# Kernel tuning notes

Hardware: AMD Instinct MI355X
Metric: run time of the kernel (lower is better)

Reference implementation:

```python
import jax, jax.numpy as jnp
import numpy as np

DIM = 2048
N_HEADS = 16
N_KV = 4
HEAD_DIM = DIM // N_HEADS  # 128
G = N_HEADS // N_KV        # queries per kv head
EPS = 1e-6
ROPE_BASE = 10000.0


def _rms_norm(x, w):
    # x: [..., head_dim]
    norm = jax.lax.rsqrt(jnp.mean(x * x, axis=-1, keepdims=True) + EPS)
    return x * norm * w


def _rope_tables(seq_len, dtype):
    inv_freq = 1.0 / (ROPE_BASE ** (jnp.arange(0, HEAD_DIM, 2, dtype=jnp.float32) / HEAD_DIM))
    t = jnp.arange(seq_len, dtype=jnp.float32)
    freqs = jnp.einsum('i,j->ij', t, inv_freq)          # [S, hd/2]
    emb = jnp.concatenate([freqs, freqs], axis=-1)       # [S, hd]
    return jnp.cos(emb).astype(dtype), jnp.sin(emb).astype(dtype)


def _rotate_half(x):
    x1, x2 = x[..., : HEAD_DIM // 2], x[..., HEAD_DIM // 2:]
    return jnp.concatenate([-x2, x1], axis=-1)


def setup_inputs() -> dict:
    key = jax.random.key(0)
    ks = jax.random.split(key, 7)
    x = jax.random.normal(ks[0], (2, 2048, DIM), dtype=jnp.float32)
    s = 0.02
    Wq = jax.random.normal(ks[1], (DIM, DIM), dtype=jnp.float32) * s
    Wk = jax.random.normal(ks[2], (DIM, N_KV * HEAD_DIM), dtype=jnp.float32) * s
    Wv = jax.random.normal(ks[3], (DIM, N_KV * HEAD_DIM), dtype=jnp.float32) * s
    Wo = jax.random.normal(ks[4], (DIM, DIM), dtype=jnp.float32) * s
    q_norm_w = jnp.ones((HEAD_DIM,), dtype=jnp.float32)
    k_norm_w = jnp.ones((HEAD_DIM,), dtype=jnp.float32)
    return {"x": x, "Wq": Wq, "Wk": Wk, "Wv": Wv, "Wo": Wo,
            "q_norm_w": q_norm_w, "k_norm_w": k_norm_w}


def reference(x, Wq, Wk, Wv, Wo, q_norm_w, k_norm_w):
    B, S, _ = x.shape
    q = (x @ Wq).reshape(B, S, N_HEADS, HEAD_DIM)
    k = (x @ Wk).reshape(B, S, N_KV, HEAD_DIM)
    v = (x @ Wv).reshape(B, S, N_KV, HEAD_DIM)

    q = _rms_norm(q, q_norm_w)
    k = _rms_norm(k, k_norm_w)

    q = q.transpose(0, 2, 1, 3)  # [B, H, S, hd]
    k = k.transpose(0, 2, 1, 3)  # [B, KV, S, hd]
    v = v.transpose(0, 2, 1, 3)

    cos, sin = _rope_tables(S, x.dtype)  # [S, hd], broadcasts over B,H
    q = q * cos + _rotate_half(q) * sin
    k = k * cos + _rotate_half(k) * sin

    # GQA: group queries by kv head instead of repeating K/V (same math as repeat_interleave)
    qg = q.reshape(B, N_KV, G, S, HEAD_DIM)
    scale = HEAD_DIM ** -0.5
    scores = jnp.einsum('bkgqd,bkkd2->bkgqk2'.replace('k2', 'K').replace('d2', 'd'),
                        qg, k) if False else jnp.einsum('bkgqd,bkKd->bkgqK', qg, k) * scale
    attn = jax.nn.softmax(scores, axis=-1)               # [B, KV, G, S, S]
    out = jnp.einsum('bkgqK,bkKd->bkgqd', attn, v)       # [B, KV, G, S, hd]
    out = out.reshape(B, N_HEADS, S, HEAD_DIM).transpose(0, 2, 1, 3).reshape(B, S, DIM)
    return out @ Wo
```

## Files before the change

kernel.cpp:

```cpp
#include <hip/hip_runtime.h>
#include <stdint.h>

#define LOG2E 1.4426950408889634f

typedef __attribute__((ext_vector_type(8))) short short8;
typedef __attribute__((ext_vector_type(4))) float floatx4;
typedef unsigned int u32;

__device__ __forceinline__ float bf2f(unsigned short h) {
  union { unsigned int u; float f; } v; v.u = ((unsigned int)h) << 16; return v.f;
}
__device__ __forceinline__ unsigned short f2bf(float f) {
  union { float f; unsigned int u; } v; v.f = f;
  unsigned int r = v.u + 0x7FFFu + ((v.u >> 16) & 1u);
  return (unsigned short)(r >> 16);
}
__device__ __forceinline__ u32 fbits(float f) {
  union { float f; u32 u; } v; v.f = f; return v.u;
}
__device__ __forceinline__ void async16(void* lds, const void* g) {
  __builtin_amdgcn_global_load_lds((const __attribute__((address_space(1))) u32*)g,
                                   (__attribute__((address_space(3))) u32*)lds, 16, 0, 0);
}

__global__ __launch_bounds__(256) void prep1(const float* __restrict__ x,
                                             const float* __restrict__ Wq,
                                             const float* __restrict__ Wk,
                                             const float* __restrict__ Wv,
                                             const float* __restrict__ Wo,
                                             unsigned short* __restrict__ xbf,
                                             unsigned short* __restrict__ WTqkv,
                                             unsigned short* __restrict__ WoT) {
  __shared__ unsigned short tile[64][65];
  int bid = blockIdx.x;
  if (bid < 4096) {
    int i = (bid * 256 + threadIdx.x) * 8;
    float4 a = ((const float4*)(x + i))[0];
    float4 b = ((const float4*)(x + i))[1];
    union { uint4 v; unsigned short u[8]; } o;
    o.u[0] = f2bf(a.x); o.u[1] = f2bf(a.y); o.u[2] = f2bf(a.z); o.u[3] = f2bf(a.w);
    o.u[4] = f2bf(b.x); o.u[5] = f2bf(b.y); o.u[6] = f2bf(b.z); o.u[7] = f2bf(b.w);
    *(uint4*)(xbf + i) = o.v;
    return;
  }
  bid -= 4096;
  const int R = 2048;
  const float* src; unsigned short* dst; int C;
  if (bid < 1024) { src = Wq; dst = WTqkv; C = 2048; }
  else if (bid < 1280) { src = Wk; dst = WTqkv + (size_t)2048 * 2048; C = 512; bid -= 1024; }
  else if (bid < 1536) { src = Wv; dst = WTqkv + (size_t)2048 * 2048 + (size_t)512 * 2048; C = 512; bid -= 1280; }
  else { src = Wo; dst = WoT; C = 2048; bid -= 1536; }

  int tc = C >> 6;
  int br = bid / tc, bc = bid % tc;
  int r0 = br << 6, c0 = bc << 6;
  int i = threadIdx.x >> 2, cc = (threadIdx.x & 3) << 4;
  const float4* g = (const float4*)(src + (size_t)(r0 + i) * C + c0 + cc);
  float4 f0 = g[0], f1 = g[1], f2 = g[2], f3 = g[3];
  unsigned short u[16];
  u[0]=f2bf(f0.x); u[1]=f2bf(f0.y); u[2]=f2bf(f0.z); u[3]=f2bf(f0.w);
  u[4]=f2bf(f1.x); u[5]=f2bf(f1.y); u[6]=f2bf(f1.z); u[7]=f2bf(f1.w);
  u[8]=f2bf(f2.x); u[9]=f2bf(f2.y); u[10]=f2bf(f2.z); u[11]=f2bf(f2.w);
  u[12]=f2bf(f3.x); u[13]=f2bf(f3.y); u[14]=f2bf(f3.z); u[15]=f2bf(f3.w);
#pragma unroll
  for (int j = 0; j < 16; ++j) tile[i][cc + j] = u[j];
  __syncthreads();
  union { uint4 v[2]; unsigned short u[16]; } buf;
#pragma unroll
  for (int j = 0; j < 16; ++j) buf.u[j] = tile[cc + j][i];
  uint4* o = (uint4*)(dst + (size_t)(c0 + i) * R + r0 + cc);
  o[0] = buf.v[0]; o[1] = buf.v[1];
}

template <typename OutT>
__global__ __launch_bounds__(512, 2) void gemm_nt_256(const unsigned short* __restrict__ A,
                                                      const unsigned short* __restrict__ BT,
                                                      OutT* __restrict__ C,
                                                      int M, int N, int K) {
  (void)M;
  __shared__ unsigned short As[2][256 * 64];
  __shared__ unsigned short Bs[2][256 * 64];
  const int nbn = N >> 8;
  const int nwg = gridDim.x;
  int wg = blockIdx.x;
  {
    int cpx = nwg >> 3;
    wg = (wg & 7) * cpx + (wg >> 3);
  }
  const int m0 = (wg / nbn) << 8;
  const int n0 = (wg % nbn) << 8;
  const int tid = threadIdx.x;
  const int lane = tid & 63, wave = tid >> 6;
  const int l15 = lane & 15, quad = lane >> 4;
  const int wr = wave >> 2, wc = wave & 3;
  const int rA = wr * 128 + l15;
  const int rB = wc * 64 + l15;

  floatx4 acc[8][4];
#pragma unroll
  for (int i = 0; i < 8; ++i)
#pragma unroll
    for (int j = 0; j < 4; ++j) acc[i][j] = (floatx4){0.f, 0.f, 0.f, 0.f};

  const unsigned short* Ag = A + (size_t)m0 * K;
  const unsigned short* Bg = BT + (size_t)n0 * K;

  auto STAGE = [&](unsigned short* dst, const unsigned short* g, int h) {
#pragma unroll
    for (int j = 0; j < 2; ++j) {
      int idx = j * 512 + tid;
      int row = h * 128 + (idx >> 3);
      int cl = (idx & 7) ^ (row & 7);
      async16(dst + (size_t)h * 8192 + (size_t)idx * 8, g + (size_t)row * K + cl * 8);
    }
  };
  auto RD = [&](const unsigned short* buf, int row, int ks) -> short8 {
    int sc = ((ks << 2) + quad) ^ (row & 7);
    return *(const short8*)(buf + row * 64 + sc * 8);
  };

#define BAR() __builtin_amdgcn_s_barrier()
#define WAITL0() asm volatile("s_waitcnt lgkmcnt(0)" ::: "memory")

  STAGE(As[0], Ag, 0); STAGE(As[0], Ag, 1);
  STAGE(Bs[0], Bg, 0); STAGE(Bs[0], Bg, 1);
  STAGE(As[1], Ag + 64, 0); STAGE(As[1], Ag + 64, 1);
  asm volatile("s_waitcnt vmcnt(4)" ::: "memory");
  BAR();

  const int NT = K >> 6;
  short8 a0[4][2], a1[4][2], b0[2][2], b1[2][2];
  for (int t = 0; t < NT; ++t) {
    const unsigned short* Ac = As[t & 1];
    const unsigned short* Bc = Bs[t & 1];
    unsigned short* Ast = As[t & 1];
    unsigned short* Bst = Bs[(t + 1) & 1];

#pragma unroll
    for (int mf = 0; mf < 4; ++mf)
#pragma unroll
      for (int ks = 0; ks < 2; ++ks) a0[mf][ks] = RD(Ac, rA + mf * 16, ks);
#pragma unroll
    for (int nf = 0; nf < 2; ++nf)
#pragma unroll
      for (int ks = 0; ks < 2; ++ks) b0[nf][ks] = RD(Bc, rB + nf * 16, ks);
    if (t + 1 < NT) STAGE(Bst, Bg + (size_t)(t + 1) * 64, 0);
    asm volatile("s_waitcnt lgkmcnt(8)" ::: "memory");
    BAR(); WAITL0();
    __builtin_amdgcn_s_setprio(1);
#pragma unroll
    for (int mf = 0; mf < 4; ++mf)
#pragma unroll
      for (int nf = 0; nf < 2; ++nf)
#pragma unroll
        for (int ks = 0; ks < 2; ++ks)
          acc[mf][nf] = __builtin_amdgcn_mfma_f32_16x16x32_bf16(a0[mf][ks], b0[nf][ks], acc[mf][nf], 0, 0, 0);
    __builtin_amdgcn_s_setprio(0);
    BAR();

#pragma unroll
    for (int mf = 0; mf < 4; ++mf)
#pragma unroll
      for (int ks = 0; ks < 2; ++ks) a1[mf][ks] = RD(Ac, rA + 64 + mf * 16, ks);
    if (t + 1 < NT) STAGE(Bst, Bg + (size_t)(t + 1) * 64, 1);
    BAR(); WAITL0();
    __builtin_amdgcn_s_setprio(1);
#pragma unroll
    for (int mf = 0; mf < 4; ++mf)
#pragma unroll
      for (int nf = 0; nf < 2; ++nf)
#pragma unroll
        for (int ks = 0; ks < 2; ++ks)
          acc[4 + mf][nf] = __builtin_amdgcn_mfma_f32_16x16x32_bf16(a1[mf][ks], b0[nf][ks], acc[4 + mf][nf], 0, 0, 0);
    __builtin_amdgcn_s_setprio(0);
    BAR();

#pragma unroll
    for (int nf = 0; nf < 2; ++nf)
#pragma unroll
      for (int ks = 0; ks < 2; ++ks) b1[nf][ks] = RD(Bc, rB + 32 + nf * 16, ks);
    if (t + 2 < NT) STAGE(Ast, Ag + (size_t)(t + 2) * 64, 0);
    BAR(); WAITL0();
    __builtin_amdgcn_s_setprio(1);
#pragma unroll
    for (int mf = 0; mf < 4; ++mf)
#pragma unroll
      for (int nf = 0; nf < 2; ++nf)
#pragma unroll
        for (int ks = 0; ks < 2; ++ks)
          acc[4 + mf][2 + nf] = __builtin_amdgcn_mfma_f32_16x16x32_bf16(a1[mf][ks], b1[nf][ks], acc[4 + mf][2 + nf], 0, 0, 0);
    __builtin_amdgcn_s_setprio(0);
    BAR();

    if (t + 2 < NT) {
      STAGE(Ast, Ag + (size_t)(t + 2) * 64, 1);
      asm volatile("s_waitcnt vmcnt(4)" ::: "memory");
    } else {
      asm volatile("s_waitcnt vmcnt(0)" ::: "memory");
    }
    BAR();
    __builtin_amdgcn_s_setprio(1);
#pragma unroll
    for (int mf = 0; mf < 4; ++mf)
#pragma unroll
      for (int nf = 0; nf < 2; ++nf)
#pragma unroll
        for (int ks = 0; ks < 2; ++ks)
          acc[mf][2 + nf] = __builtin_amdgcn_mfma_f32_16x16x32_bf16(a0[mf][ks], b1[nf][ks], acc[mf][2 + nf], 0, 0, 0);
    __builtin_amdgcn_s_setprio(0);
    BAR();
  }
#undef BAR
#undef WAITL0

#pragma unroll
  for (int mf = 0; mf < 8; ++mf)
#pragma unroll
    for (int nf = 0; nf < 4; ++nf)
#pragma unroll
      for (int r = 0; r < 4; ++r) {
        int m = m0 + wr * 128 + mf * 16 + quad * 4 + r;
        int n = n0 + wc * 64 + nf * 16 + l15;
        float v = acc[mf][nf][r];
        if constexpr (sizeof(OutT) == 2)
          C[(size_t)m * N + n] = (OutT)f2bf(v);
        else
          C[(size_t)m * N + n] = (OutT)v;
      }
}

__global__ __launch_bounds__(512, 2) void gemm_nt_128x256(const unsigned short* __restrict__ A,
                                                          const unsigned short* __restrict__ BT,
                                                          float* __restrict__ C,
                                                          int M, int N, int K) {
  (void)M;
  __shared__ unsigned short As[2][128 * 64];
  __shared__ unsigned short Bs[2][256 * 64];
  const int nbn = N >> 8;
  const int nwg = gridDim.x;
  int wg = blockIdx.x;
  {
    int cpx = nwg >> 3;
    wg = (wg & 7) * cpx + (wg >> 3);
  }
  const int m0 = (wg / nbn) << 7;
  const int n0 = (wg % nbn) << 8;
  const int tid = threadIdx.x;
  const int lane = tid & 63, wave = tid >> 6;
  const int l15 = lane & 15, quad = lane >> 4;
  const int wr = wave >> 2, wc = wave & 3;
  const int rA = wr * 64 + l15;
  const int rB = wc * 64 + l15;

  floatx4 acc[4][4];
#pragma unroll
  for (int i = 0; i < 4; ++i)
#pragma unroll
    for (int j = 0; j < 4; ++j) acc[i][j] = (floatx4){0.f, 0.f, 0.f, 0.f};

  const unsigned short* Ag = A + (size_t)m0 * K;
  const unsigned short* Bg = BT + (size_t)n0 * K;

  auto STAGE_B = [&](unsigned short* dst, const unsigned short* g, int h) {
#pragma unroll
    for (int j = 0; j < 2; ++j) {
      int idx = j * 512 + tid;
      int row = h * 128 + (idx >> 3);
      int cl = (idx & 7) ^ (row & 7);
      async16(dst + (size_t)h * 8192 + (size_t)idx * 8, g + (size_t)row * K + cl * 8);
    }
  };
  auto STAGE_A = [&](unsigned short* dst, const unsigned short* g, int h) {
    int idx = tid;
    int row = h * 64 + (idx >> 3);
    int cl = (idx & 7) ^ (row & 7);
    async16(dst + (size_t)h * 4096 + (size_t)idx * 8, g + (size_t)row * K + cl * 8);
  };
  auto RD = [&](const unsigned short* buf, int row, int ks) -> short8 {
    int sc = ((ks << 2) + quad) ^ (row & 7);
    return *(const short8*)(buf + row * 64 + sc * 8);
  };

#define BAR() __builtin_amdgcn_s_barrier()
#define WAITL0() asm volatile("s_waitcnt lgkmcnt(0)" ::: "memory")

  STAGE_A(As[0], Ag, 0); STAGE_A(As[0], Ag, 1);
  STAGE_B(Bs[0], Bg, 0); STAGE_B(Bs[0], Bg, 1);
  STAGE_A(As[1], Ag + 64, 0); STAGE_A(As[1], Ag + 64, 1);
  asm volatile("s_waitcnt vmcnt(2)" ::: "memory");
  BAR();

  const int NT = K >> 6;
  short8 a0[2][2], a1[2][2], b0[2][2], b1[2][2];
  for (int t = 0; t < NT; ++t) {
    const unsigned short* Ac = As[t & 1];
    const unsigned short* Bc = Bs[t & 1];
    unsigned short* Ast = As[t & 1];
    unsigned short* Bst = Bs[(t + 1) & 1];

#pragma unroll
    for (int mf = 0; mf < 2; ++mf)
#pragma unroll
      for (int ks = 0; ks < 2; ++ks) a0[mf][ks] = RD(Ac, rA + mf * 16, ks);
#pragma unroll
    for (int nf = 0; nf < 2; ++nf)
#pragma unroll
      for (int ks = 0; ks < 2; ++ks) b0[nf][ks] = RD(Bc, rB + nf * 16, ks);
    if (t + 1 < NT) STAGE_B(Bst, Bg + (size_t)(t + 1) * 64, 0);
    asm volatile("s_waitcnt lgkmcnt(4)" ::: "memory");
    BAR(); WAITL0();
    __builtin_amdgcn_s_setprio(1);
#pragma unroll
    for (int mf = 0; mf < 2; ++mf)
#pragma unroll
      for (int nf = 0; nf < 2; ++nf)
#pragma unroll
        for (int ks = 0; ks < 2; ++ks)
          acc[mf][nf] = __builtin_amdgcn_mfma_f32_16x16x32_bf16(a0[mf][ks], b0[nf][ks], acc[mf][nf], 0, 0, 0);
    __builtin_amdgcn_s_setprio(0);
    BAR();

#pragma unroll
    for (int mf = 0; mf < 2; ++mf)
#pragma unroll
      for (int ks = 0; ks < 2; ++ks) a1[mf][ks] = RD(Ac, rA + 32 + mf * 16, ks);
    if (t + 1 < NT) STAGE_B(Bst, Bg + (size_t)(t + 1) * 64, 1);
    BAR(); WAITL0();
    __builtin_amdgcn_s_setprio(1);
#pragma unroll
    for (int mf = 0; mf < 2; ++mf)
#pragma unroll
      for (int nf = 0; nf < 2; ++nf)
#pragma unroll
        for (int ks = 0; ks < 2; ++ks)
          acc[2 + mf][nf] = __builtin_amdgcn_mfma_f32_16x16x32_bf16(a1[mf][ks], b0[nf][ks], acc[2 + mf][nf], 0, 0, 0);
    __builtin_amdgcn_s_setprio(0);
    BAR();

#pragma unroll
    for (int nf = 0; nf < 2; ++nf)
#pragma unroll
      for (int ks = 0; ks < 2; ++ks) b1[nf][ks] = RD(Bc, rB + 32 + nf * 16, ks);
    if (t + 2 < NT) STAGE_A(Ast, Ag + (size_t)(t + 2) * 64, 0);
    BAR(); WAITL0();
    __builtin_amdgcn_s_setprio(1);
#pragma unroll
    for (int mf = 0; mf < 2; ++mf)
#pragma unroll
      for (int nf = 0; nf < 2; ++nf)
#pragma unroll
        for (int ks = 0; ks < 2; ++ks)
          acc[2 + mf][2 + nf] = __builtin_amdgcn_mfma_f32_16x16x32_bf16(a1[mf][ks], b1[nf][ks], acc[2 + mf][2 + nf], 0, 0, 0);
    __builtin_amdgcn_s_setprio(0);
    BAR();

    if (t + 2 < NT) {
      STAGE_A(Ast, Ag + (size_t)(t + 2) * 64, 1);
      asm volatile("s_waitcnt vmcnt(2)" ::: "memory");
    } else {
      asm volatile("s_waitcnt vmcnt(0)" ::: "memory");
    }
    BAR();
    __builtin_amdgcn_s_setprio(1);
#pragma unroll
    for (int mf = 0; mf < 2; ++mf)
#pragma unroll
      for (int nf = 0; nf < 2; ++nf)
#pragma unroll
        for (int ks = 0; ks < 2; ++ks)
          acc[mf][2 + nf] = __builtin_amdgcn_mfma_f32_16x16x32_bf16(a0[mf][ks], b1[nf][ks], acc[mf][2 + nf], 0, 0, 0);
    __builtin_amdgcn_s_setprio(0);
    BAR();
  }
#undef BAR
#undef WAITL0

#pragma unroll
  for (int mf = 0; mf < 4; ++mf)
#pragma unroll
    for (int nf = 0; nf < 4; ++nf)
#pragma unroll
      for (int r = 0; r < 4; ++r) {
        int m = m0 + wr * 64 + mf * 16 + quad * 4 + r;
        int n = n0 + wc * 64 + nf * 16 + l15;
        C[(size_t)m * N + n] = acc[mf][nf][r];
      }
}

__global__ __launch_bounds__(256) void prep2(const unsigned short* __restrict__ qkv,
                                             const float* __restrict__ qw,
                                             const float* __restrict__ kw,
                                             unsigned short* __restrict__ qT,
                                             unsigned short* __restrict__ kT,
                                             unsigned short* __restrict__ vT) {
  const int S = 2048;
  __shared__ unsigned short tile[64][65];
  int bid = blockIdx.x;
  if (bid < 2048) {
    int wave = threadIdx.x >> 6, lane = threadIdx.x & 63;
    int wid0 = bid * 4 + wave;
    float ifr = exp2f((float)lane * -0.2076205059304601f);
    const float qwl1 = qw[lane], qwl2 = qw[lane + 64];
    const float kwl1 = kw[lane], kwl2 = kw[lane + 64];
    for (int k = 0; k < 10; ++k) {
      int wid = wid0 + k * 8192;
      int slot = wid % 20;
      int bs = wid / 20;
      int s = bs & (S - 1), b = bs >> 11;
      const unsigned short* src;
      unsigned short* dst;
      float w1, w2, scale;
      if (slot < 16) {
        src = qkv + (size_t)bs * 3072 + slot * 128;
        dst = qT + ((size_t)(b * 16 + slot) * S + s) * 128;
        w1 = qwl1; w2 = qwl2;
        scale = 0.08838834764831845f * 1.4426950408889634f;
      } else {
        int kvi = slot - 16;
        src = qkv + (size_t)bs * 3072 + 2048 + kvi * 128;
        dst = kT + ((size_t)(b * 4 + kvi) * S + s) * 128;
        w1 = kwl1; w2 = kwl2;
        scale = 1.0f;
      }
      float x1 = bf2f(src[lane]), x2 = bf2f(src[lane + 64]);
      float ss = x1 * x1 + x2 * x2;
#pragma unroll
      for (int m = 1; m < 64; m <<= 1) ss += __shfl_xor(ss, m, 64);
      float rms = rsqrtf(ss * (1.0f / 128.0f) + 1e-6f);
      float y1 = x1 * rms * w1;
      float y2 = x2 * rms * w2;
      float ang = (float)s * ifr;
      float c = cosf(ang), sn = sinf(ang);
      float o1 = (y1 * c - y2 * sn) * scale;
      float o2 = (y2 * c + y1 * sn) * scale;
      dst[lane] = f2bf(o1);
      dst[lane + 64] = f2bf(o2);
    }
    return;
  }
  bid -= 2048;
  int dt = bid & 1, st = (bid >> 1) & 31, kv = (bid >> 6) & 3, b = bid >> 8;
  int s0 = st << 6, d0 = dt << 6;
  int i = threadIdx.x >> 2, cc = (threadIdx.x & 3) << 4;
  union { uint4 v[2]; unsigned short u[16]; } buf;
  const uint4* g = (const uint4*)(qkv + ((size_t)(b * S) + s0 + i) * 3072 + 2560 + kv * 128 + d0 + cc);
  buf.v[0] = g[0]; buf.v[1] = g[1];
#pragma unroll
  for (int j = 0; j < 16; ++j) tile[i][cc + j] = buf.u[j];
  __syncthreads();
#pragma unroll
  for (int j = 0; j < 16; ++j) buf.u[j] = tile[cc + j][i];
  uint4* o = (uint4*)(vT + ((size_t)(b * 4 + kv) * 128 + d0 + i) * S + s0 + cc);
  o[0] = buf.v[0]; o[1] = buf.v[1];
}

__global__ __launch_bounds__(256, 2) void flash_attn(const unsigned short* __restrict__ qT,
                                                     const unsigned short* __restrict__ kT,
                                                     const unsigned short* __restrict__ vT,
                                                     unsigned short* __restrict__ ao) {
  const int S = 2048;
  int bid = blockIdx.x;
  int qt = bid & 15, h = (bid >> 4) & 15, b = bid >> 8;
  int kv = h >> 2;
  int tid = threadIdx.x;
  int lane = tid & 63, wave = tid >> 6;
  int l15 = lane & 15, quad = lane >> 4;

  __shared__ unsigned short Ks[2][64 * 128];
  __shared__ unsigned short VTs[2][128 * 64];
  __shared__ unsigned short Ps[4][32 * 64];
  unsigned short* Psw = Ps[wave];

  short8 bq[2][4];
  const unsigned short* qbase = qT + ((size_t)(b * 16 + h) * S + qt * 128 + wave * 32) * 128;
#pragma unroll
  for (int nt = 0; nt < 2; ++nt)
#pragma unroll
    for (int kk = 0; kk < 4; ++kk)
      bq[nt][kk] = *(const short8*)(qbase + (size_t)(nt * 16 + l15) * 128 + kk * 32 + quad * 8);

  floatx4 O[2][8];
#pragma unroll
  for (int mt = 0; mt < 2; ++mt)
#pragma unroll
    for (int dt = 0; dt < 8; ++dt) O[mt][dt] = (floatx4){0.f, 0.f, 0.f, 0.f};
  float l_acc[2] = {0.f, 0.f};

  const size_t kbase = (size_t)(b * 4 + kv) * S * 128;
  const size_t vbase = (size_t)(b * 4 + kv) * 128 * S;

#pragma unroll
  for (int i = 0; i < 4; ++i) {
    int Lc = (wave * 4 + i) * 64 + lane;
    int row = Lc >> 4, cjk = (lane & 15) ^ (row & 7);
    async16(Ks[0] + (size_t)Lc * 8, kT + kbase + (size_t)row * 128 + cjk * 8);
    int d = Lc >> 3, cjv = (lane & 7) ^ (d & 7);
    async16(VTs[0] + (size_t)Lc * 8, vT + vbase + (size_t)d * S + cjv * 8);
  }

  for (int kt = 0; kt < 32; ++kt) {
    int cur = kt & 1;
    __syncthreads();
    if (kt + 1 < 32) {
#pragma unroll
      for (int i = 0; i < 4; ++i) {
        int Lc = (wave * 4 + i) * 64 + lane;
        int row = Lc >> 4, cjk = (lane & 15) ^ (row & 7);
        async16(Ks[cur ^ 1] + (size_t)Lc * 8,
                kT + kbase + (size_t)((kt + 1) * 64 + row) * 128 + cjk * 8);
        int d = Lc >> 3, cjv = (lane & 7) ^ (d & 7);
        async16(VTs[cur ^ 1] + (size_t)Lc * 8,
                vT + vbase + (size_t)d * S + (kt + 1) * 64 + cjv * 8);
      }
    }

    floatx4 st[4][2];
#pragma unroll
    for (int a = 0; a < 4; ++a)
#pragma unroll
      for (int nt = 0; nt < 2; ++nt) st[a][nt] = (floatx4){0.f, 0.f, 0.f, 0.f};
    __builtin_amdgcn_s_setprio(1);
#pragma unroll
    for (int kk = 0; kk < 4; ++kk)
#pragma unroll
      for (int a = 0; a < 4; ++a) {
        int m = a * 16 + l15;
        short8 ak = *(const short8*)(&Ks[cur][(m * 16 + ((kk * 4 + quad) ^ (m & 7))) * 8]);
#pragma unroll
        for (int nt = 0; nt < 2; ++nt)
          st[a][nt] = __builtin_amdgcn_mfma_f32_16x16x32_bf16(ak, bq[nt][kk], st[a][nt], 0, 0, 0);
      }
    __builtin_amdgcn_s_setprio(0);

#pragma unroll
    for (int nt = 0; nt < 2; ++nt) {
      int m = nt * 16 + l15;
#pragma unroll
      for (int a = 0; a < 4; ++a) {
        float e0 = __builtin_amdgcn_exp2f(st[a][nt][0]);
        float e1 = __builtin_amdgcn_exp2f(st[a][nt][1]);
        float e2 = __builtin_amdgcn_exp2f(st[a][nt][2]);
        float e3 = __builtin_amdgcn_exp2f(st[a][nt][3]);
        l_acc[nt] += (e0 + e1) + (e2 + e3);
        u32 p01 = __builtin_amdgcn_perm(fbits(e1) + 0x8000u, fbits(e0) + 0x8000u, 0x07060302u);
        u32 p23 = __builtin_amdgcn_perm(fbits(e3) + 0x8000u, fbits(e2) + 0x8000u, 0x07060302u);
        int c = (a * 2 + (quad >> 1)) ^ (m & 7);
        uint2 pk; pk.x = p01; pk.y = p23;
        *(uint2*)(&Psw[(m * 8 + c) * 8 + (quad & 1) * 4]) = pk;
      }
    }

    __builtin_amdgcn_s_setprio(1);
#pragma unroll
    for (int kk2 = 0; kk2 < 2; ++kk2) {
      short8 ap[2];
#pragma unroll
      for (int mt = 0; mt < 2; ++mt) {
        int m = mt * 16 + l15;
        ap[mt] = *(const short8*)(&Psw[(m * 8 + ((kk2 * 4 + quad) ^ (m & 7))) * 8]);
      }
#pragma unroll
      for (int dt = 0; dt < 8; ++dt) {
        int n = dt * 16 + l15;
        short8 bv = *(const short8*)(&VTs[cur][(n * 8 + ((kk2 * 4 + quad) ^ (n & 7))) * 8]);
#pragma unroll
        for (int mt = 0; mt < 2; ++mt)
          O[mt][dt] = __builtin_amdgcn_mfma_f32_16x16x32_bf16(ap[mt], bv, O[mt][dt], 0, 0, 0);
      }
    }
    __builtin_amdgcn_s_setprio(0);
  }

  float linv[2];
#pragma unroll
  for (int nt = 0; nt < 2; ++nt) {
    float l = l_acc[nt];
    l += __shfl_xor(l, 16, 64);
    l += __shfl_xor(l, 32, 64);
    linv[nt] = 1.f / l;
  }
#pragma unroll
  for (int mt = 0; mt < 2; ++mt)
#pragma unroll
    for (int r = 0; r < 4; ++r) {
      float inv = __shfl(linv[mt], quad * 4 + r, 64);
      int s = qt * 128 + wave * 32 + mt * 16 + quad * 4 + r;
#pragma unroll
      for (int dt = 0; dt < 8; ++dt) {
        int d = dt * 16 + l15;
        ao[((size_t)(b * S + s) * 16 + h) * 128 + d] = f2bf(O[mt][dt][r] * inv);
      }
    }
}

extern "C" void kernel_launch(void* const* d_in, const int* in_sizes, int n_in,
                              void* d_out, int out_size, void* d_ws, size_t ws_size,
                              hipStream_t stream) {
  const float* x  = (const float*)d_in[0];
  const float* Wq = (const float*)d_in[1];
  const float* Wk = (const float*)d_in[2];
  const float* Wv = (const float*)d_in[3];
  const float* Wo = (const float*)d_in[4];
  const float* qw = (const float*)d_in[5];
  const float* kw = (const float*)d_in[6];
  float* out = (float*)d_out;

  unsigned short* p = (unsigned short*)d_ws;
  unsigned short* xbf   = p; p += (size_t)4096 * 2048;
  unsigned short* WTqkv = p; p += (size_t)3072 * 2048;
  unsigned short* WoT   = p; p += (size_t)2048 * 2048;
  unsigned short* qkv   = p; p += (size_t)4096 * 3072;
  unsigned short* qTb   = p; p += (size_t)2 * 16 * 2048 * 128;
  unsigned short* kTb   = p; p += (size_t)2 * 4 * 2048 * 128;
  unsigned short* vTb   = p; p += (size_t)2 * 4 * 2048 * 128;
  unsigned short* ao    = p; p += (size_t)4096 * 2048;

  prep1<<<6656, 256, 0, stream>>>(x, Wq, Wk, Wv, Wo, xbf, WTqkv, WoT);

  gemm_nt_256<unsigned short><<<192, 512, 0, stream>>>(xbf, WTqkv, qkv, 4096, 3072, 2048);

  prep2<<<2560, 256, 0, stream>>>(qkv, qw, kw, qTb, kTb, vTb);

  flash_attn<<<512, 256, 0, stream>>>(qTb, kTb, vTb, ao);

  gemm_nt_128x256<<<256, 512, 0, stream>>>(ao, WoT, out, 4096, 2048, 2048);
}
```

Baseline: 321.1 us.

## Use 256x192 tiles for QKV GEMM to fill all CUs

Changes the QKV projection GEMM tile from 256x256 to 256x192 so the grid grows from 192 to 256 workgroups, better matching the CU count. B staging is rewritten as a single 3-load stage per K-step, and each wave now computes three 16-wide N fragments instead of four. This aims to reduce idle CUs and tail imbalance, at the cost of lower per-tile arithmetic intensity and changed overlap of B loads with compute.

```diff
diff --git a/kernel.cpp b/kernel.cpp
--- a/kernel.cpp
+++ b/kernel.cpp
@@ -72,15 +72,14 @@
   o[0] = buf.v[0]; o[1] = buf.v[1];
 }
 
-template <typename OutT>
-__global__ __launch_bounds__(512, 2) void gemm_nt_256(const unsigned short* __restrict__ A,
-                                                      const unsigned short* __restrict__ BT,
-                                                      OutT* __restrict__ C,
-                                                      int M, int N, int K) {
+__global__ __launch_bounds__(512, 2) void gemm_nt_256x192(const unsigned short* __restrict__ A,
+                                                          const unsigned short* __restrict__ BT,
+                                                          unsigned short* __restrict__ C,
+                                                          int M, int N, int K) {
   (void)M;
   __shared__ unsigned short As[2][256 * 64];
-  __shared__ unsigned short Bs[2][256 * 64];
-  const int nbn = N >> 8;
+  __shared__ unsigned short Bs[2][192 * 64];
+  const int nbn = N / 192;
   const int nwg = gridDim.x;
   int wg = blockIdx.x;
   {
@@ -88,24 +87,24 @@
     wg = (wg & 7) * cpx + (wg >> 3);
   }
   const int m0 = (wg / nbn) << 8;
-  const int n0 = (wg % nbn) << 8;
+  const int n0 = (wg % nbn) * 192;
   const int tid = threadIdx.x;
   const int lane = tid & 63, wave = tid >> 6;
   const int l15 = lane & 15, quad = lane >> 4;
   const int wr = wave >> 2, wc = wave & 3;
   const int rA = wr * 128 + l15;
-  const int rB = wc * 64 + l15;
-
-  floatx4 acc[8][4];
+  const int rB = wc * 48 + l15;
+
+  floatx4 acc[8][3];
 #pragma unroll
   for (int i = 0; i < 8; ++i)
 #pragma unroll
-    for (int j = 0; j < 4; ++j) acc[i][j] = (floatx4){0.f, 0.f, 0.f, 0.f};
+    for (int j = 0; j < 3; ++j) acc[i][j] = (floatx4){0.f, 0.f, 0.f, 0.f};
 
   const unsigned short* Ag = A + (size_t)m0 * K;
   const unsigned short* Bg = BT + (size_t)n0 * K;
 
-  auto STAGE = [&](unsigned short* dst, const unsigned short* g, int h) {
+  auto STAGE_A = [&](unsigned short* dst, const unsigned short* g, int h) {
 #pragma unroll
     for (int j = 0; j < 2; ++j) {
       int idx = j * 512 + tid;
@@ -114,6 +113,15 @@
       async16(dst + (size_t)h * 8192 + (size_t)idx * 8, g + (size_t)row * K + cl * 8);
     }
   };
+  auto STAGE_B = [&](unsigned short* dst, const unsigned short* g) {
+#pragma unroll
+    for (int j = 0; j < 3; ++j) {
+      int idx = j * 512 + tid;
+      int row = idx >> 3;
+      int cl = (idx & 7) ^ (row & 7);
+      async16(dst + (size_t)idx * 8, g + (size_t)row * K + cl * 8);
+    }
+  };
   auto RD = [&](const unsigned short* buf, int row, int ks) -> short8 {
     int sc = ((ks << 2) + quad) ^ (row & 7);
     return *(const short8*)(buf + row * 64 + sc * 8);
@@ -122,14 +130,14 @@
 #define BAR() __builtin_amdgcn_s_barrier()
 #define WAITL0() asm volatile("s_waitcnt lgkmcnt(0)" ::: "memory")
 
-  STAGE(As[0], Ag, 0); STAGE(As[0], Ag, 1);
-  STAGE(Bs[0], Bg, 0); STAGE(Bs[0], Bg, 1);
-  STAGE(As[1], Ag + 64, 0); STAGE(As[1], Ag + 64, 1);
+  STAGE_A(As[0], Ag, 0); STAGE_A(As[0], Ag, 1);
+  STAGE_B(Bs[0], Bg);
+  STAGE_A(As[1], Ag + 64, 0); STAGE_A(As[1], Ag + 64, 1);
   asm volatile("s_waitcnt vmcnt(4)" ::: "memory");
   BAR();
 
   const int NT = K >> 6;
-  short8 a0[4][2], a1[4][2], b0[2][2], b1[2][2];
+  short8 a0[4][2], a1[4][2], b0[2][2], b1[2];
   for (int t = 0; t < NT; ++t) {
     const unsigned short* Ac = As[t & 1];
     const unsigned short* Bc = Bs[t & 1];
@@ -144,7 +152,7 @@
     for (int nf = 0; nf < 2; ++nf)
 #pragma unroll
       for (int ks = 0; ks < 2; ++ks) b0[nf][ks] = RD(Bc, rB + nf * 16, ks);
-    if (t + 1 < NT) STAGE(Bst, Bg + (size_t)(t + 1) * 64, 0);
+    if (t + 1 < NT) STAGE_B(Bst, Bg + (size_t)(t + 1) * 64);
     asm volatile("s_waitcnt lgkmcnt(8)" ::: "memory");
     BAR(); WAITL0();
     __builtin_amdgcn_s_setprio(1);
@@ -162,7 +170,6 @@
     for (int mf = 0; mf < 4; ++mf)
 #pragma unroll
       for (int ks = 0; ks < 2; ++ks) a1[mf][ks] = RD(Ac, rA + 64 + mf * 16, ks);
-    if (t + 1 < NT) STAGE(Bst, Bg + (size_t)(t + 1) * 64, 1);
     BAR(); WAITL0();
     __builtin_amdgcn_s_setprio(1);
 #pragma unroll
@@ -176,24 +183,20 @@
     BAR();
 
 #pragma unroll
-    for (int nf = 0; nf < 2; ++nf)
-#pragma unroll
-      for (int ks = 0; ks < 2; ++ks) b1[nf][ks] = RD(Bc, rB + 32 + nf * 16, ks);
-    if (t + 2 < NT) STAGE(Ast, Ag + (size_t)(t + 2) * 64, 0);
+    for (int ks = 0; ks < 2; ++ks) b1[ks] = RD(Bc, rB + 32, ks);
+    if (t + 2 < NT) STAGE_A(Ast, Ag + (size_t)(t + 2) * 64, 0);
     BAR(); WAITL0();
     __builtin_amdgcn_s_setprio(1);
 #pragma unroll
     for (int mf = 0; mf < 4; ++mf)
 #pragma unroll
-      for (int nf = 0; nf < 2; ++nf)
-#pragma unroll
-        for (int ks = 0; ks < 2; ++ks)
-          acc[4 + mf][2 + nf] = __builtin_amdgcn_mfma_f32_16x16x32_bf16(a1[mf][ks], b1[nf][ks], acc[4 + mf][2 + nf], 0, 0, 0);
+      for (int ks = 0; ks < 2; ++ks)
+        acc[4 + mf][2] = __builtin_amdgcn_mfma_f32_16x16x32_bf16(a1[mf][ks], b1[ks], acc[4 + mf][2], 0, 0, 0);
     __builtin_amdgcn_s_setprio(0);
     BAR();
 
     if (t + 2 < NT) {
-      STAGE(Ast, Ag + (size_t)(t + 2) * 64, 1);
+      STAGE_A(Ast, Ag + (size_t)(t + 2) * 64, 1);
       asm volatile("s_waitcnt vmcnt(4)" ::: "memory");
     } else {
       asm volatile("s_waitcnt vmcnt(0)" ::: "memory");
@@ -203,10 +206,8 @@
 #pragma unroll
     for (int mf = 0; mf < 4; ++mf)
 #pragma unroll
-      for (int nf = 0; nf < 2; ++nf)
-#pragma unroll
-        for (int ks = 0; ks < 2; ++ks)
-          acc[mf][2 + nf] = __builtin_amdgcn_mfma_f32_16x16x32_bf16(a0[mf][ks], b1[nf][ks], acc[mf][2 + nf], 0, 0, 0);
+      for (int ks = 0; ks < 2; ++ks)
+        acc[mf][2] = __builtin_amdgcn_mfma_f32_16x16x32_bf16(a0[mf][ks], b1[ks], acc[mf][2], 0, 0, 0);
     __builtin_amdgcn_s_setprio(0);
     BAR();
   }
@@ -216,16 +217,12 @@
 #pragma unroll
   for (int mf = 0; mf < 8; ++mf)
 #pragma unroll
-    for (int nf = 0; nf < 4; ++nf)
+    for (int nf = 0; nf < 3; ++nf)
 #pragma unroll
       for (int r = 0; r < 4; ++r) {
         int m = m0 + wr * 128 + mf * 16 + quad * 4 + r;
-        int n = n0 + wc * 64 + nf * 16 + l15;
-        float v = acc[mf][nf][r];
-        if constexpr (sizeof(OutT) == 2)
-          C[(size_t)m * N + n] = (OutT)f2bf(v);
-        else
-          C[(size_t)m * N + n] = (OutT)v;
+        int n = n0 + wc * 48 + nf * 16 + l15;
+        C[(size_t)m * N + n] = f2bf(acc[mf][nf][r]);
       }
 }
 
@@ -617,7 +614,7 @@
 
   prep1<<<6656, 256, 0, stream>>>(x, Wq, Wk, Wv, Wo, xbf, WTqkv, WoT);
 
-  gemm_nt_256<unsigned short><<<192, 512, 0, stream>>>(xbf, WTqkv, qkv, 4096, 3072, 2048);
+  gemm_nt_256x192<<<256, 512, 0, stream>>>(xbf, WTqkv, qkv, 4096, 3072, 2048);
 
   prep2<<<2560, 256, 0, stream>>>(qkv, qw, kw, qTb, kTb, vTb);
 
```

After: 309.9 us, median of 2. 1.04x faster.
